# Kernel optimization log

Measured on AMD Instinct MI355X. Metric: run time of the kernel, lower is better.

The kernel has to match this reference:

```python
import jax, jax.numpy as jnp
import numpy as np

B, T, E = 4, 2048, 256
H = 8
HD = E // H
FE = 4
L = 4
EPS = 1e-5


def _layernorm(x, g, b):
    mu = jnp.mean(x, axis=-1, keepdims=True)
    var = jnp.mean((x - mu) ** 2, axis=-1, keepdims=True)
    return (x - mu) * jax.lax.rsqrt(var + EPS) * g + b


def setup_inputs() -> dict:
    key = jax.random.key(0)
    ks = jax.random.split(key, 14)
    s = 0.02
    inp = {
        "x": jax.random.normal(ks[0], (B, T, E), dtype=jnp.float32),
        "qkv_w": jax.random.normal(ks[1], (L, E, 3 * E), dtype=jnp.float32) * s,
        "qkv_b": jnp.zeros((L, 3 * E), jnp.float32),
        "out_w": jax.random.normal(ks[2], (L, E, E), dtype=jnp.float32) * s,
        "out_b": jnp.zeros((L, E), jnp.float32),
        "ff1_w": jax.random.normal(ks[3], (L, E, FE * E), dtype=jnp.float32) * s,
        "ff1_b": jnp.zeros((L, FE * E), jnp.float32),
        "ff2_w": jax.random.normal(ks[4], (L, FE * E, E), dtype=jnp.float32) * s,
        "ff2_b": jnp.zeros((L, E), jnp.float32),
        "ln1_g": jnp.ones((L, E), jnp.float32),
        "ln1_b": jnp.zeros((L, E), jnp.float32),
        "ln2_g": jnp.ones((L, E), jnp.float32),
        "ln2_b": jnp.zeros((L, E), jnp.float32),
    }
    return inp


def _fourier_pe(x):
    # freqs over even indices: 10000^(-i/E), i = 0,2,...,E-2  -> E/2 freqs
    freqs = jnp.power(10000.0, -jnp.arange(0, E, 2, dtype=jnp.float32) / E)
    pos = jnp.arange(T, dtype=jnp.float32)[:, None]          # (T,1)
    sinusoid = pos * freqs[None, :]                            # (T, E/2)
    pe = jnp.concatenate([jnp.sin(sinusoid), jnp.cos(sinusoid)], axis=-1)  # (T,E)
    return x + pe[None, :, :]


def _forward(x, qkv_w, qkv_b, out_w, out_b, ff1_w, ff1_b, ff2_w, ff2_b,
             ln1_g, ln1_b, ln2_g, ln2_b):
    x = _fourier_pe(x)
    scale = 1.0 / np.sqrt(HD)
    for i in range(L):
        # attention (dropout = identity at eval)
        qkv = x @ qkv_w[i] + qkv_b[i]                          # (B,T,3E)
        qkv = qkv.reshape(B, T, H, 3, HD)                      # chunk of 3*hd -> (3,hd)
        q, k, v = qkv[..., 0, :], qkv[..., 1, :], qkv[..., 2, :]  # (B,T,H,HD)
        scores = jnp.einsum("bqhd,bkhd->bhqk", q, k) * scale   # (B,H,T,T)
        w = jax.nn.softmax(scores, axis=-1)
        attn = jnp.einsum("bhqk,bkhd->bqhd", w, v).reshape(B, T, E)
        attn = attn @ out_w[i] + out_b[i]
        x = _layernorm(x + attn, ln1_g[i], ln1_b[i])
        # feedforward
        h = jax.nn.relu(x @ ff1_w[i] + ff1_b[i])
        ff = h @ ff2_w[i] + ff2_b[i]
        x = _layernorm(x + ff, ln2_g[i], ln2_b[i])
    return x


def reference(x, qkv_w, qkv_b, out_w, out_b, ff1_w, ff1_b, ff2_w, ff2_b,
              ln1_g, ln1_b, ln2_g, ln2_b):
    return _forward(x, qkv_w, qkv_b, out_w, out_b, ff1_w, ff1_b, ff2_w, ff2_b,
                    ln1_g, ln1_b, ln2_g, ln2_b)
```

## Files before the change

kernel.cpp:

```cpp
#include <hip/hip_runtime.h>
#include <hip/hip_bf16.h>
#include <stdint.h>

typedef unsigned short u16;
typedef _Float16 f16;
typedef short vs8 __attribute__((ext_vector_type(8)));
typedef float vf4 __attribute__((ext_vector_type(4)));
typedef _Float16 vh2 __attribute__((ext_vector_type(2)));
typedef _Float16 vh4 __attribute__((ext_vector_type(4)));
typedef _Float16 vh8 __attribute__((ext_vector_type(8)));
typedef __fp16 hw2 __attribute__((ext_vector_type(2)));


__device__ __forceinline__ void gload16(const u16* g, u16* l) {
  __builtin_amdgcn_global_load_lds((const __attribute__((address_space(1))) void*)g,
                                   (__attribute__((address_space(3))) void*)l,
                                   16, 0, 0);
}

__device__ __forceinline__ float fexp2(float x) {
#if __has_builtin(__builtin_amdgcn_exp2f)
  return __builtin_amdgcn_exp2f(x);
#else
  return __expf(x * 0.69314718056f);
#endif
}

__global__ void pe_kernel(const float* __restrict__ x, __hip_bfloat16* __restrict__ Xb) {
  int row = blockIdx.x;
  int e = threadIdx.x;
  int t = row & 2047;
  int f = (e < 128) ? e : (e - 128);
  float freq = powf(10000.0f, -(float)f * (1.0f / 128.0f));
  float arg = (float)t * freq;
  float pe = (e < 128) ? sinf(arg) : cosf(arg);
  size_t idx = (size_t)row * 256 + e;
  Xb[idx] = __float2bfloat16(x[idx] + pe);
}

__global__ void transpose_cast(const float* __restrict__ in, u16* __restrict__ out,
                               int K, int N) {
  __shared__ float tile[32][33];
  int layer = blockIdx.z;
  int k0 = blockIdx.x * 32, n0 = blockIdx.y * 32;
  const float* ip = in + (size_t)layer * K * N;
  u16* op = out + (size_t)layer * N * K;
  int tx = threadIdx.x, ty = threadIdx.y;
#pragma unroll
  for (int r = 0; r < 4; ++r) {
    int k = ty + r * 8;
    tile[k][tx] = ip[(size_t)(k0 + k) * N + (n0 + tx)];
  }
  __syncthreads();
#pragma unroll
  for (int r = 0; r < 4; ++r) {
    int n = ty + r * 8;
    __hip_bfloat16 v = __float2bfloat16(tile[tx][n]);
    op[(size_t)(n0 + n) * K + (k0 + tx)] = *(u16*)&v;
  }
}

__global__ __launch_bounds__(256, 2) void gemm_relu(
    const u16* __restrict__ A, const u16* __restrict__ Bt,
    const float* __restrict__ bias, __hip_bfloat16* __restrict__ outB,
    int M, int N, int K) {
  __shared__ u16 As[128 * 32];
  __shared__ u16 Bs[128 * 32];
  int tid = threadIdx.x;
  int wave = tid >> 6, lane = tid & 63;
  int wm = wave & 1, wn = wave >> 1;
  int m0 = blockIdx.y * 128, n0 = blockIdx.x * 128;
  int lr = lane & 15, lq = lane >> 4;

  vf4 acc[4][4];
#pragma unroll
  for (int i = 0; i < 4; ++i)
#pragma unroll
    for (int j = 0; j < 4; ++j) {
      acc[i][j][0] = 0.f; acc[i][j][1] = 0.f; acc[i][j][2] = 0.f; acc[i][j][3] = 0.f;
    }

  int srow = wave * 16 + (lane >> 2);
  int scol = (lane & 3) * 8;
  const u16* ag = A + (size_t)(m0 + srow) * K + scol;
  const u16* bg = Bt + (size_t)(n0 + srow) * K + scol;
  u16* al = As + srow * 32 + scol;
  u16* bl = Bs + srow * 32 + scol;
  const size_t rstride = (size_t)64 * K;

  for (int k0 = 0; k0 < K; k0 += 32) {
    gload16(ag + k0, al);
    gload16(ag + k0 + rstride, al + 64 * 32);
    gload16(bg + k0, bl);
    gload16(bg + k0 + rstride, bl + 64 * 32);
    __syncthreads();
    vs8 av[4], bv[4];
#pragma unroll
    for (int i = 0; i < 4; ++i)
      av[i] = *(const vs8*)&As[(wm * 64 + i * 16 + lr) * 32 + lq * 8];
#pragma unroll
    for (int j = 0; j < 4; ++j)
      bv[j] = *(const vs8*)&Bs[(wn * 64 + j * 16 + lr) * 32 + lq * 8];
#pragma unroll
    for (int i = 0; i < 4; ++i)
#pragma unroll
      for (int j = 0; j < 4; ++j)
        acc[i][j] = __builtin_amdgcn_mfma_f32_16x16x32_bf16(av[i], bv[j], acc[i][j], 0, 0, 0);
    __syncthreads();
  }

#pragma unroll
  for (int i = 0; i < 4; ++i) {
    int row0 = m0 + wm * 64 + i * 16 + lq * 4;
#pragma unroll
    for (int j = 0; j < 4; ++j) {
      int col = n0 + wn * 64 + j * 16 + lr;
      float bb = bias[col];
#pragma unroll
      for (int r = 0; r < 4; ++r) {
        size_t idx = (size_t)(row0 + r) * N + col;
        outB[idx] = __float2bfloat16(fmaxf(acc[i][j][r] + bb, 0.0f));
      }
    }
  }
}

__global__ __launch_bounds__(256, 2) void gemm_qkv(
    const u16* __restrict__ A, const u16* __restrict__ Bt,
    const float* __restrict__ bias, f16* __restrict__ outH,
    int M, int N, int K) {
  __shared__ u16 As[64 * 32];
  __shared__ u16 Bs[128 * 32];
  int tid = threadIdx.x;
  int wave = tid >> 6, lane = tid & 63;
  int wm = wave & 1, wn = wave >> 1;
  int m0 = blockIdx.y * 64, n0 = blockIdx.x * 128;
  int lr = lane & 15, lq = lane >> 4;

  vf4 acc[2][4];
#pragma unroll
  for (int i = 0; i < 2; ++i)
#pragma unroll
    for (int j = 0; j < 4; ++j) { acc[i][j][0]=0.f; acc[i][j][1]=0.f; acc[i][j][2]=0.f; acc[i][j][3]=0.f; }

  int sr = tid >> 2, sc = (tid & 3) * 8;
  const u16* ag = A + (size_t)(m0 + sr) * K + sc;
  const u16* bg = Bt + (size_t)(n0 + sr) * K + sc;
  u16* al = As + sr * 32 + sc;
  u16* bl = Bs + sr * 32 + sc;

  for (int k0 = 0; k0 < K; k0 += 32) {
    gload16(ag + k0, al);
    gload16(bg + k0, bl);
    gload16(bg + k0 + (size_t)64 * K, bl + 64 * 32);
    __syncthreads();
    vs8 av[2], bv[4];
#pragma unroll
    for (int i = 0; i < 2; ++i)
      av[i] = *(const vs8*)&As[(wm * 32 + i * 16 + lr) * 32 + lq * 8];
#pragma unroll
    for (int j = 0; j < 4; ++j)
      bv[j] = *(const vs8*)&Bs[(wn * 64 + j * 16 + lr) * 32 + lq * 8];
#pragma unroll
    for (int i = 0; i < 2; ++i)
#pragma unroll
      for (int j = 0; j < 4; ++j)
        acc[i][j] = __builtin_amdgcn_mfma_f32_16x16x32_bf16(av[i], bv[j], acc[i][j], 0, 0, 0);
    __syncthreads();
  }

#pragma unroll
  for (int i = 0; i < 2; ++i) {
    int row0 = m0 + wm * 32 + i * 16 + lq * 4;
#pragma unroll
    for (int j = 0; j < 4; ++j) {
      int col = n0 + wn * 64 + j * 16 + lr;
      float bb = bias[col];
#pragma unroll
      for (int r = 0; r < 4; ++r)
        outH[(size_t)(row0 + r) * N + col] = (f16)(acc[i][j][r] + bb);
    }
  }
}

__global__ __launch_bounds__(512, 2) void gemm_ln(
    const u16* __restrict__ A, const u16* __restrict__ Bt,
    const float* __restrict__ bias, const __hip_bfloat16* __restrict__ res,
    const float* __restrict__ gam, const float* __restrict__ bet,
    __hip_bfloat16* __restrict__ outB, float* __restrict__ outF, int K) {
  __shared__ u16 As[32 * 32];
  __shared__ u16 Bs[256 * 32];
  __shared__ float ps[4][32], ps2[4][32], mur[32], rsr[32];
  int tid = threadIdx.x;
  int wave = tid >> 6, lane = tid & 63;
  int wm = wave & 1, wn = wave >> 1;
  int lr = lane & 15, lq = lane >> 4;
  int m0 = blockIdx.x * 32;

  vf4 acc[4];
#pragma unroll
  for (int j = 0; j < 4; ++j) { acc[j][0]=0.f; acc[j][1]=0.f; acc[j][2]=0.f; acc[j][3]=0.f; }

  int sr = tid >> 2, sc = (tid & 3) * 8;
  const u16* ag = A + (size_t)(m0 + sr) * K + sc;
  const u16* bg = Bt + (size_t)sr * K + sc;
  u16* al = As + sr * 32 + sc;
  u16* bl = Bs + sr * 32 + sc;

  for (int k0 = 0; k0 < K; k0 += 32) {
    if (tid < 128) gload16(ag + k0, al);
    gload16(bg + k0, bl);
    gload16(bg + k0 + (size_t)128 * K, bl + 128 * 32);
    __syncthreads();
    vs8 av, bv[4];
    av = *(const vs8*)&As[(wm * 16 + lr) * 32 + lq * 8];
#pragma unroll
    for (int j = 0; j < 4; ++j)
      bv[j] = *(const vs8*)&Bs[(wn * 64 + j * 16 + lr) * 32 + lq * 8];
#pragma unroll
    for (int j = 0; j < 4; ++j)
      acc[j] = __builtin_amdgcn_mfma_f32_16x16x32_bf16(av, bv[j], acc[j], 0, 0, 0);
    __syncthreads();
  }

  float sum_[4], sq_[4];
#pragma unroll
  for (int r = 0; r < 4; ++r) { sum_[r] = 0.f; sq_[r] = 0.f; }
#pragma unroll
  for (int j = 0; j < 4; ++j) {
    int col = wn * 64 + j * 16 + lr;
    float bb = bias[col];
#pragma unroll
    for (int r = 0; r < 4; ++r) {
      int row = m0 + wm * 16 + lq * 4 + r;
      float v = acc[j][r] + bb + __bfloat162float(res[(size_t)row * 256 + col]);
      acc[j][r] = v;
      sum_[r] += v;
      sq_[r] += v * v;
    }
  }
#pragma unroll
  for (int r = 0; r < 4; ++r) {
#pragma unroll
    for (int m = 1; m <= 8; m <<= 1) {
      sum_[r] += __shfl_xor(sum_[r], m);
      sq_[r]  += __shfl_xor(sq_[r], m);
    }
  }
  if (lr == 0) {
#pragma unroll
    for (int r = 0; r < 4; ++r) {
      int rl = wm * 16 + lq * 4 + r;
      ps[wn][rl] = sum_[r];
      ps2[wn][rl] = sq_[r];
    }
  }
  __syncthreads();
  if (tid < 32) {
    float s = ps[0][tid] + ps[1][tid] + ps[2][tid] + ps[3][tid];
    float s2 = ps2[0][tid] + ps2[1][tid] + ps2[2][tid] + ps2[3][tid];
    float mu = s * (1.0f / 256.0f);
    float var = s2 * (1.0f / 256.0f) - mu * mu;
    mur[tid] = mu;
    rsr[tid] = rsqrtf(var + 1e-5f);
  }
  __syncthreads();
#pragma unroll
  for (int r = 0; r < 4; ++r) {
    int rl = wm * 16 + lq * 4 + r;
    float mu = mur[rl], rs = rsr[rl];
    int row = m0 + rl;
#pragma unroll
    for (int j = 0; j < 4; ++j) {
      int col = wn * 64 + j * 16 + lr;
      float o = (acc[j][r] - mu) * rs * gam[col] + bet[col];
      size_t idx = (size_t)row * 256 + col;
      outB[idx] = __float2bfloat16(o);
      if (outF) outF[idx] = o;
    }
  }
}

__global__ __launch_bounds__(512, 4) void attn_mfma(const f16* __restrict__ qkv,
                                                    __hip_bfloat16* __restrict__ out) {
  __shared__ __align__(16) u16 lds[2][9344];
  int tid = threadIdx.x;
  int wave = tid >> 6, lane = tid & 63;
  int lr = lane & 15, quad = lane >> 4;

  int id = blockIdx.x;
  int xcd = id & 7, slot = id >> 3;
  int grp = xcd * 4 + (slot & 3);
  int qt = slot >> 2;
  int b = grp >> 3, h = grp & 7;
  int q0 = qt * 256;
  int rowbase = b * 2048;
  const f16* base_bh = qkv + (size_t)rowbase * 768 + h * 96;

  vh8 qf[2];
#pragma unroll
  for (int nt = 0; nt < 2; ++nt) {
    int qr = q0 + wave * 32 + nt * 16 + lr;
    vh8 t = *(const vh8*)(base_bh + (size_t)qr * 768 + quad * 8);
#pragma unroll
    for (int j = 0; j < 8; ++j) t[j] = t[j] * (f16)0.25508682f;
    qf[nt] = t;
  }

  vf4 O[2][2], lO[2];
#pragma unroll
  for (int a = 0; a < 2; ++a) {
    lO[a][0]=0.f; lO[a][1]=0.f; lO[a][2]=0.f; lO[a][3]=0.f;
#pragma unroll
    for (int d = 0; d < 2; ++d) { O[a][d][0]=0.f; O[a][d][1]=0.f; O[a][d][2]=0.f; O[a][d][3]=0.f; }
  }

  int srK = tid >> 2;
  int scK = (tid & 3) * 8;
  const f16* kg = base_bh + (size_t)srK * 768 + 32 + scK;
  int kvp = tid >> 3;
  int d4 = (tid & 7) * 4;
  const f16* vg = base_bh + (size_t)(kvp * 2) * 768 + 64 + d4;

  const vf4 z4 = {0.f, 0.f, 0.f, 0.f};
  const vh4 onesh = {(f16)1.0f, (f16)1.0f, (f16)1.0f, (f16)1.0f};
  const size_t cstep = (size_t)128 * 768;

  {
    vh8 k0 = *(const vh8*)kg;
    *(vh8*)&lds[0][srK * 40 + scK] = k0;
    vh4 a = *(const vh4*)vg;
    vh4 bb = *(const vh4*)(vg + 768);
    f16* vt0 = (f16*)&lds[0][5120];
#pragma unroll
    for (int i = 0; i < 4; ++i) {
      vh2 pr; pr[0] = a[i]; pr[1] = bb[i];
      *(vh2*)(vt0 + (d4 + i) * 132 + kvp * 2) = pr;
    }
  }
  __syncthreads();

  for (int c = 0; c < 16; ++c) {
    int cur = c & 1;
    const f16* Ks = (const f16*)&lds[cur][0];
    const f16* VT = (const f16*)&lds[cur][5120];

    vh8 kn; vh4 va, vb;
    if (c < 15) {
      kn = *(const vh8*)(kg + (size_t)(c + 1) * cstep);
      const f16* vp = vg + (size_t)(c + 1) * cstep;
      va = *(const vh4*)vp;
      vb = *(const vh4*)(vp + 768);
    }

#pragma unroll
    for (int t16 = 0; t16 < 8; ++t16) {
      vh8 ak = *(const vh8*)&Ks[(t16 * 16 + lr) * 40 + quad * 8];
      vf4 s0 = __builtin_amdgcn_mfma_f32_16x16x32_f16(ak, qf[0], z4, 0, 0, 0);
      vf4 s1 = __builtin_amdgcn_mfma_f32_16x16x32_f16(ak, qf[1], z4, 0, 0, 0);
      vh4 p0, p1;
      ((hw2*)&p0)[0] = __builtin_amdgcn_cvt_pkrtz(fexp2(s0[0]), fexp2(s0[1]));
      ((hw2*)&p0)[1] = __builtin_amdgcn_cvt_pkrtz(fexp2(s0[2]), fexp2(s0[3]));
      ((hw2*)&p1)[0] = __builtin_amdgcn_cvt_pkrtz(fexp2(s1[0]), fexp2(s1[1]));
      ((hw2*)&p1)[1] = __builtin_amdgcn_cvt_pkrtz(fexp2(s1[2]), fexp2(s1[3]));
      vh4 vf0 = *(const vh4*)&VT[(0 * 16 + lr) * 132 + t16 * 16 + quad * 4];
      vh4 vf1 = *(const vh4*)&VT[(1 * 16 + lr) * 132 + t16 * 16 + quad * 4];
      O[0][0] = __builtin_amdgcn_mfma_f32_16x16x16f16(p0, vf0, O[0][0], 0, 0, 0);
      O[0][1] = __builtin_amdgcn_mfma_f32_16x16x16f16(p0, vf1, O[0][1], 0, 0, 0);
      O[1][0] = __builtin_amdgcn_mfma_f32_16x16x16f16(p1, vf0, O[1][0], 0, 0, 0);
      O[1][1] = __builtin_amdgcn_mfma_f32_16x16x16f16(p1, vf1, O[1][1], 0, 0, 0);
      lO[0] = __builtin_amdgcn_mfma_f32_16x16x16f16(p0, onesh, lO[0], 0, 0, 0);
      lO[1] = __builtin_amdgcn_mfma_f32_16x16x16f16(p1, onesh, lO[1], 0, 0, 0);
    }

    if (c < 15) {
      *(vh8*)&lds[cur ^ 1][srK * 40 + scK] = kn;
      f16* vt1 = (f16*)&lds[cur ^ 1][5120];
#pragma unroll
      for (int i = 0; i < 4; ++i) {
        vh2 pr; pr[0] = va[i]; pr[1] = vb[i];
        *(vh2*)(vt1 + (d4 + i) * 132 + kvp * 2) = pr;
      }
    }
    __syncthreads();
  }

#pragma unroll
  for (int nt = 0; nt < 2; ++nt) {
#pragma unroll
    for (int r = 0; r < 4; ++r) {
      float inv = 1.0f / lO[nt][r];
      int row = rowbase + q0 + wave * 32 + nt * 16 + quad * 4 + r;
#pragma unroll
      for (int dt = 0; dt < 2; ++dt) {
        int col = h * 32 + dt * 16 + lr;
        out[(size_t)row * 256 + col] = __float2bfloat16(O[nt][dt][r] * inv);
      }
    }
  }
}

extern "C" void kernel_launch(void* const* d_in, const int* in_sizes, int n_in,
                              void* d_out, int out_size, void* d_ws, size_t ws_size,
                              hipStream_t stream) {
  (void)in_sizes; (void)n_in; (void)out_size; (void)ws_size;
  const float* x     = (const float*)d_in[0];
  const float* qkv_b = (const float*)d_in[2];
  const float* out_b = (const float*)d_in[4];
  const float* ff1_b = (const float*)d_in[6];
  const float* ff2_b = (const float*)d_in[8];
  const float* ln1_g = (const float*)d_in[9];
  const float* ln1_b = (const float*)d_in[10];
  const float* ln2_g = (const float*)d_in[11];
  const float* ln2_b = (const float*)d_in[12];

  char* ws = (char*)d_ws;
  __hip_bfloat16* Xb    = (__hip_bfloat16*)(ws + 8388608);
  __hip_bfloat16* attnB = (__hip_bfloat16*)(ws + 20971520);
  f16*            qkvH  = (f16*)(ws + 25165824);
  __hip_bfloat16* hB    = (__hip_bfloat16*)(ws + 20971520);
  u16* qkvwT = (u16*)(ws + 37748736);
  u16* outwT = (u16*)(ws + 39321600);
  u16* ff1wT = (u16*)(ws + 39845888);
  u16* ff2wT = (u16*)(ws + 41943040);

  pe_kernel<<<8192, 256, 0, stream>>>(x, Xb);
  transpose_cast<<<dim3(8, 24, 4), dim3(32, 8), 0, stream>>>((const float*)d_in[1], qkvwT, 256, 768);
  transpose_cast<<<dim3(8, 8, 4),  dim3(32, 8), 0, stream>>>((const float*)d_in[3], outwT, 256, 256);
  transpose_cast<<<dim3(8, 32, 4), dim3(32, 8), 0, stream>>>((const float*)d_in[5], ff1wT, 256, 1024);
  transpose_cast<<<dim3(32, 8, 4), dim3(32, 8), 0, stream>>>((const float*)d_in[7], ff2wT, 1024, 256);

  for (int l = 0; l < 4; ++l) {
    gemm_qkv<<<dim3(6, 128), 256, 0, stream>>>((const u16*)Xb, qkvwT + (size_t)l * 768 * 256,
        qkv_b + l * 768, qkvH, 8192, 768, 256);
    attn_mfma<<<256, 512, 0, stream>>>(qkvH, attnB);
    gemm_ln<<<256, 512, 0, stream>>>((const u16*)attnB, outwT + (size_t)l * 256 * 256,
        out_b + l * 256, Xb, ln1_g + l * 256, ln1_b + l * 256, Xb, nullptr, 256);
    gemm_relu<<<dim3(8, 64), 256, 0, stream>>>((const u16*)Xb, ff1wT + (size_t)l * 1024 * 256,
        ff1_b + l * 1024, hB, 8192, 1024, 256);
    float* lnout = (l == 3) ? (float*)d_out : nullptr;
    gemm_ln<<<256, 512, 0, stream>>>((const u16*)hB, ff2wT + (size_t)l * 256 * 1024,
        ff2_b + l * 256, Xb, ln2_g + l * 256, ln2_b + l * 256, Xb, lnout, 1024);
  }
}
```

Before: 456.0 us.

## Split attention KV range in two and combine partial results

```diff
diff --git a/kernel.cpp b/kernel.cpp
--- a/kernel.cpp
+++ b/kernel.cpp
@@ -282,7 +282,8 @@
 }
 
 __global__ __launch_bounds__(512, 4) void attn_mfma(const f16* __restrict__ qkv,
-                                                    __hip_bfloat16* __restrict__ out) {
+                                                    f16* __restrict__ Of,
+                                                    float* __restrict__ lf) {
   __shared__ __align__(16) u16 lds[2][9344];
   int tid = threadIdx.x;
   int wave = tid >> 6, lane = tid & 63;
@@ -291,9 +292,11 @@
   int id = blockIdx.x;
   int xcd = id & 7, slot = id >> 3;
   int grp = xcd * 4 + (slot & 3);
-  int qt = slot >> 2;
+  int qt = (slot >> 2) & 7;
+  int split = slot >> 5;
   int b = grp >> 3, h = grp & 7;
   int q0 = qt * 256;
+  int kv0 = split << 10;
   int rowbase = b * 2048;
   const f16* base_bh = qkv + (size_t)rowbase * 768 + h * 96;
 
@@ -317,10 +320,10 @@
 
   int srK = tid >> 2;
   int scK = (tid & 3) * 8;
-  const f16* kg = base_bh + (size_t)srK * 768 + 32 + scK;
+  const f16* kg = base_bh + (size_t)(kv0 + srK) * 768 + 32 + scK;
   int kvp = tid >> 3;
   int d4 = (tid & 7) * 4;
-  const f16* vg = base_bh + (size_t)(kvp * 2) * 768 + 64 + d4;
+  const f16* vg = base_bh + (size_t)(kv0 + kvp * 2) * 768 + 64 + d4;
 
   const vf4 z4 = {0.f, 0.f, 0.f, 0.f};
   const vh4 onesh = {(f16)1.0f, (f16)1.0f, (f16)1.0f, (f16)1.0f};
@@ -340,13 +343,13 @@
   }
   __syncthreads();
 
-  for (int c = 0; c < 16; ++c) {
+  for (int c = 0; c < 8; ++c) {
     int cur = c & 1;
     const f16* Ks = (const f16*)&lds[cur][0];
     const f16* VT = (const f16*)&lds[cur][5120];
 
     vh8 kn; vh4 va, vb;
-    if (c < 15) {
+    if (c < 7) {
       kn = *(const vh8*)(kg + (size_t)(c + 1) * cstep);
       const f16* vp = vg + (size_t)(c + 1) * cstep;
       va = *(const vh4*)vp;
@@ -373,7 +376,7 @@
       lO[1] = __builtin_amdgcn_mfma_f32_16x16x16f16(p1, onesh, lO[1], 0, 0, 0);
     }
 
-    if (c < 15) {
+    if (c < 7) {
       *(vh8*)&lds[cur ^ 1][srK * 40 + scK] = kn;
       f16* vt1 = (f16*)&lds[cur ^ 1][5120];
 #pragma unroll
@@ -389,15 +392,38 @@
   for (int nt = 0; nt < 2; ++nt) {
 #pragma unroll
     for (int r = 0; r < 4; ++r) {
-      float inv = 1.0f / lO[nt][r];
-      int row = rowbase + q0 + wave * 32 + nt * 16 + quad * 4 + r;
+      int tq = q0 + wave * 32 + nt * 16 + quad * 4 + r;
+      if (lr == 0) lf[split * 65536 + grp * 2048 + tq] = lO[nt][r];
+      int row = rowbase + tq;
 #pragma unroll
       for (int dt = 0; dt < 2; ++dt) {
         int col = h * 32 + dt * 16 + lr;
-        out[(size_t)row * 256 + col] = __float2bfloat16(O[nt][dt][r] * inv);
+        Of[(size_t)split * 2097152 + (size_t)row * 256 + col] = (f16)O[nt][dt][r];
       }
     }
   }
+}
+
+__global__ __launch_bounds__(256) void attn_combine(const f16* __restrict__ Of,
+                                                    const float* __restrict__ lf,
+                                                    __hip_bfloat16* __restrict__ out) {
+  int idx = blockIdx.x * 256 + threadIdx.x;
+  int row = idx >> 5;
+  int col0 = (idx & 31) * 8;
+  int grp = ((row >> 11) << 3) + (col0 >> 5);
+  int t = row & 2047;
+  float l = lf[grp * 2048 + t] + lf[65536 + grp * 2048 + t];
+  float inv = 1.0f / l;
+  size_t off = (size_t)row * 256 + col0;
+  vh8 a = *(const vh8*)(Of + off);
+  vh8 bq = *(const vh8*)(Of + 2097152 + off);
+  union { vs8 v; u16 u[8]; } o;
+#pragma unroll
+  for (int j = 0; j < 8; ++j) {
+    __hip_bfloat16 hb = __float2bfloat16(((float)a[j] + (float)bq[j]) * inv);
+    o.u[j] = *(u16*)&hb;
+  }
+  *(vs8*)((u16*)out + off) = o.v;
 }
 
 extern "C" void kernel_launch(void* const* d_in, const int* in_sizes, int n_in,
@@ -415,7 +441,9 @@
   const float* ln2_b = (const float*)d_in[12];
 
   char* ws = (char*)d_ws;
+  f16*            Of    = (f16*)(ws + 0);
   __hip_bfloat16* Xb    = (__hip_bfloat16*)(ws + 8388608);
+  float*          lf    = (float*)(ws + 12582912);
   __hip_bfloat16* attnB = (__hip_bfloat16*)(ws + 20971520);
   f16*            qkvH  = (f16*)(ws + 25165824);
   __hip_bfloat16* hB    = (__hip_bfloat16*)(ws + 20971520);
@@ -433,7 +461,8 @@
   for (int l = 0; l < 4; ++l) {
     gemm_qkv<<<dim3(6, 128), 256, 0, stream>>>((const u16*)Xb, qkvwT + (size_t)l * 768 * 256,
         qkv_b + l * 768, qkvH, 8192, 768, 256);
-    attn_mfma<<<256, 512, 0, stream>>>(qkvH, attnB);
+    attn_mfma<<<512, 512, 0, stream>>>(qkvH, Of, lf);
+    attn_combine<<<1024, 256, 0, stream>>>(Of, lf, attnB);
     gemm_ln<<<256, 512, 0, stream>>>((const u16*)attnB, outwT + (size_t)l * 256 * 256,
         out_b + l * 256, Xb, ln1_g + l * 256, ln1_b + l * 256, Xb, nullptr, 256);
     gemm_relu<<<dim3(8, 64), 256, 0, stream>>>((const u16*)Xb, ff1wT + (size_t)l * 1024 * 256,
```

Measured after the change: 463.4 us. About the same (+1.6%).
